# Kernel tuning notes

Measured on AMD Instinct MI355X. Metric: run time of the kernel, lower is better.

Reference implementation:

```python
import jax, jax.numpy as jnp
import numpy as np

B, S, N_WIRES, EMBED_DIM, NUM_HEADS = 4, 2048, 8, 512, 8
D_K = EMBED_DIM // NUM_HEADS


def setup_inputs() -> dict:
    key = jax.random.key(0)
    k_x, k_th, k_q, k_k, k_v, k_c = jax.random.split(key, 6)
    x = jax.random.normal(k_x, (B, S, N_WIRES), dtype=jnp.float32)
    # trainable RX rotation angles, one per wire
    theta = jax.random.normal(k_th, (N_WIRES,), dtype=jnp.float32) * 0.1
    # nn.Linear(n_wires, embed_dim, bias=False) weights have shape (embed_dim, n_wires)
    sc_in = 1.0 / np.sqrt(N_WIRES)
    Wq = jax.random.normal(k_q, (EMBED_DIM, N_WIRES), dtype=jnp.float32) * sc_in
    Wk = jax.random.normal(k_k, (EMBED_DIM, N_WIRES), dtype=jnp.float32) * sc_in
    Wv = jax.random.normal(k_v, (EMBED_DIM, N_WIRES), dtype=jnp.float32) * sc_in
    Wc = jax.random.normal(k_c, (EMBED_DIM, EMBED_DIM), dtype=jnp.float32) * (1.0 / np.sqrt(EMBED_DIM))
    return {"x": x, "theta": theta, "Wq": Wq, "Wk": Wk, "Wv": Wv, "Wc": Wc}


def reference(x, theta, Wq, Wk, Wv, Wc):
    # Quantum encoding closed form: RX(x_i) then RX(theta_i) on |0> per wire gives <Z> = cos(x_i + theta_i).
    proj = jnp.cos(x + theta)  # (B, S, n_wires)
    b, s, _ = proj.shape
    q = jnp.einsum('bsn,en->bse', proj, Wq)
    k = jnp.einsum('bsn,en->bse', proj, Wk)
    v = jnp.einsum('bsn,en->bse', proj, Wv)
    # split heads: (B, H, S, d_k)
    q = q.reshape(b, s, NUM_HEADS, D_K).transpose(0, 2, 1, 3)
    k = k.reshape(b, s, NUM_HEADS, D_K).transpose(0, 2, 1, 3)
    v = v.reshape(b, s, NUM_HEADS, D_K).transpose(0, 2, 1, 3)
    scores = jnp.einsum('bhqd,bhkd->bhqk', q, k) / np.sqrt(D_K).astype(np.float32)
    attn = jax.nn.softmax(scores, axis=-1)  # dropout is identity at inference
    out = jnp.einsum('bhqk,bhkd->bhqd', attn, v)
    out = out.transpose(0, 2, 1, 3).reshape(b, s, EMBED_DIM)
    return jnp.einsum('bse,fe->bsf', out, Wc)
```

## Files before the change

kernel.cpp:

```cpp
#include <hip/hip_runtime.h>
#include <stdint.h>

#define N_B 4
#define S_LEN 2048
#define N_H 8
#define E_DIM 512

typedef __attribute__((ext_vector_type(8))) short bf16x8;
typedef __attribute__((ext_vector_type(4))) float f32x4;
typedef __attribute__((ext_vector_type(4))) unsigned int u32x4;
typedef __attribute__((ext_vector_type(2))) unsigned int u32x2;
typedef __attribute__((ext_vector_type(4))) unsigned short u16x4;
typedef __attribute__((ext_vector_type(8))) unsigned short u16x8;

#define MFMA16(a, b, c) __builtin_amdgcn_mfma_f32_16x16x32_bf16((a), (b), (c), 0, 0, 0)

__device__ __forceinline__ unsigned short f2bf(float f) {
    union { float f; unsigned int u; } v; v.f = f;
    unsigned int r = v.u + 0x7fffu + ((v.u >> 16) & 1u);
    return (unsigned short)(r >> 16);
}

__device__ __forceinline__ unsigned int pack2bf(float lo, float hi) {
    union { float f; unsigned int u; } a, b; a.f = lo; b.f = hi;
    return __builtin_amdgcn_perm(b.u + 0x8000u, a.u + 0x8000u, 0x07060302u);
}

__device__ __forceinline__ float fexp2(float x) {
#if __has_builtin(__builtin_amdgcn_exp2f)
    return __builtin_amdgcn_exp2f(x);
#else
    return exp2f(x);
#endif
}

#if __has_builtin(__builtin_amdgcn_permlane32_swap) && __has_builtin(__builtin_amdgcn_permlane16_swap)
#define HAVE_PERMLANE_SWAP 1
#endif

__device__ __forceinline__ void pl32(unsigned int& x, unsigned int& y) {
#ifdef HAVE_PERMLANE_SWAP
    auto r = __builtin_amdgcn_permlane32_swap(x, y, false, false);
    x = (unsigned int)r[0]; y = (unsigned int)r[1];
#else
    const int idx = (((int)threadIdx.x & 63) ^ 32) << 2;
    unsigned int xs = (unsigned int)__builtin_amdgcn_ds_bpermute(idx, (int)x);
    unsigned int ys = (unsigned int)__builtin_amdgcn_ds_bpermute(idx, (int)y);
    const bool lo = (threadIdx.x & 32) == 0;
    unsigned int nx = lo ? x : ys;
    unsigned int ny = lo ? xs : y;
    x = nx; y = ny;
#endif
}

__device__ __forceinline__ void pl16(unsigned int& x, unsigned int& y) {
#ifdef HAVE_PERMLANE_SWAP
    auto r = __builtin_amdgcn_permlane16_swap(x, y, false, false);
    x = (unsigned int)r[0]; y = (unsigned int)r[1];
#else
    unsigned int zs = (unsigned int)__builtin_amdgcn_ds_swizzle((int)y, 0x401F);
    unsigned int ws = (unsigned int)__builtin_amdgcn_ds_swizzle((int)x, 0x401F);
    const bool evenq = (threadIdx.x & 16) == 0;
    unsigned int nx = evenq ? x : zs;
    unsigned int ny = evenq ? ws : y;
    x = nx; y = ny;
#endif
}

#define Q_SCALE 0.18033688f

__global__ __launch_bounds__(256) void qkv_kernel(
    const float* __restrict__ x, const float* __restrict__ theta,
    const float* __restrict__ Wq, const float* __restrict__ Wk,
    const float* __restrict__ Wv,
    unsigned short* __restrict__ Q, unsigned short* __restrict__ K,
    unsigned short* __restrict__ Vt)
{
    __shared__ float proj[32][8];
    const int tid = threadIdx.x;
    const int mat = blockIdx.x % 3;
    const int chunk = blockIdx.x / 3;
    const int row0 = chunk * 32;
    const int b = row0 >> 11;
    const int s_in_b = row0 & (S_LEN - 1);

    proj[tid >> 3][tid & 7] = cosf(x[row0 * 8 + tid] + theta[tid & 7]);
    __syncthreads();

    if (mat < 2) {
        const float* W = (mat == 0) ? Wq : Wk;
        const float scale = (mat == 0) ? Q_SCALE : 1.0f;
        unsigned short* outp = (mat == 0) ? Q : K;
        const int eg = (tid & 127) * 4;
        const int sg = (tid >> 7) * 16;
        float w[4][8];
        #pragma unroll
        for (int e = 0; e < 4; ++e)
            #pragma unroll
            for (int n = 0; n < 8; ++n)
                w[e][n] = W[(eg + e) * 8 + n] * scale;
        const int h = eg >> 6, d0 = eg & 63;
        unsigned short* p0 = outp + ((size_t)(b * N_H + h) * S_LEN + s_in_b + sg) * 64 + d0;
        #pragma unroll 4
        for (int s = 0; s < 16; ++s) {
            f32x4 pa = *(const f32x4*)&proj[sg + s][0];
            f32x4 pc = *(const f32x4*)&proj[sg + s][4];
            u16x4 o;
            #pragma unroll
            for (int e = 0; e < 4; ++e) {
                float a = 0.f;
                #pragma unroll
                for (int n = 0; n < 4; ++n)
                    a += pa[n] * w[e][n] + pc[n] * w[e][n + 4];
                o[e] = f2bf(a);
            }
            *(u16x4*)&p0[s * 64] = o;
        }
    } else {
        f32x4 ps[8][2];
        const int sl0 = (tid & 3) * 8;
        #pragma unroll
        for (int k2 = 0; k2 < 8; ++k2) {
            ps[k2][0] = *(const f32x4*)&proj[sl0 + k2][0];
            ps[k2][1] = *(const f32x4*)&proj[sl0 + k2][4];
        }
        const int ecol = tid >> 2;
        for (int pass = 0; pass < 8; ++pass) {
            const int e = pass * 64 + ecol;
            const int h = e >> 6, dd = e & 63;
            float wr[8];
            #pragma unroll
            for (int n = 0; n < 8; ++n) wr[n] = Wv[e * 8 + n];
            u16x8 pk;
            #pragma unroll
            for (int k2 = 0; k2 < 8; ++k2) {
                float acc = 0.f;
                #pragma unroll
                for (int n = 0; n < 4; ++n)
                    acc += ps[k2][0][n] * wr[n] + ps[k2][1][n] * wr[n + 4];
                pk[k2] = f2bf(acc);
            }
            *(u16x8*)&Vt[((size_t)(b * N_H + h) * 64 + dd) * S_LEN + s_in_b + sl0] = pk;
        }
    }
}

__global__ __launch_bounds__(256, 2) void flash_kernel(
    const unsigned short* __restrict__ Q, const unsigned short* __restrict__ K,
    const unsigned short* __restrict__ Vt, unsigned short* __restrict__ O)
{
    __shared__ short kt[2][64 * 72];
    __shared__ short vt[2][64 * 72];

    const int tid = threadIdx.x;
    const int lane = tid & 63, w = tid >> 6;
    const int quad = lane >> 4, lq = lane & 15;
    const int qt = blockIdx.x & 15, bh = blockIdx.x >> 4;
    const int b = bh >> 3, h = bh & 7;

    const unsigned short* Qb = Q + (size_t)bh * S_LEN * 64;
    const unsigned short* Kb = K + (size_t)bh * S_LEN * 64;
    const unsigned short* Vb = Vt + (size_t)bh * 64 * S_LEN;

    bf16x8 qf[2][2];
    #pragma unroll
    for (int mt = 0; mt < 2; ++mt)
        #pragma unroll
        for (int ks = 0; ks < 2; ++ks)
            qf[mt][ks] = *(const bf16x8*)&Qb[(size_t)(qt * 128 + w * 32 + mt * 16 + lq) * 64 + ks * 32 + quad * 8];

    f32x4 oacc[2][4];
    #pragma unroll
    for (int mt = 0; mt < 2; ++mt)
        #pragma unroll
        for (int dt = 0; dt < 4; ++dt) oacc[mt][dt] = 0.f;
    float lsum[2] = {0.f, 0.f};

    u32x4 pkr[2], pvr[2];
    #pragma unroll
    for (int i = 0; i < 2; ++i) {
        const int u = tid + (i << 8);
        pkr[i] = *(const u32x4*)&Kb[(size_t)(u >> 3) * 64 + (u & 7) * 8];
        pvr[i] = *(const u32x4*)&Vb[(size_t)(u >> 3) * S_LEN + (u & 7) * 8];
    }
    #pragma unroll
    for (int i = 0; i < 2; ++i) {
        const int u = tid + (i << 8);
        *(u32x4*)&kt[0][(u >> 3) * 72 + (u & 7) * 8] = pkr[i];
        *(u32x4*)&vt[0][(u >> 3) * 72 + (u & 7) * 8] = pvr[i];
    }
    #pragma unroll
    for (int i = 0; i < 2; ++i) {
        const int u = tid + (i << 8);
        pkr[i] = *(const u32x4*)&Kb[(size_t)(64 + (u >> 3)) * 64 + (u & 7) * 8];
        pvr[i] = *(const u32x4*)&Vb[(size_t)(u >> 3) * S_LEN + 64 + (u & 7) * 8];
    }
    asm volatile("s_waitcnt lgkmcnt(0)" ::: "memory");
    __builtin_amdgcn_s_barrier();

    for (int kti = 0; kti < 32; ++kti) {
        const int cur = kti & 1, nxt = cur ^ 1;

        #pragma unroll
        for (int i = 0; i < 2; ++i) {
            const int u = tid + (i << 8);
            *(u32x4*)&kt[nxt][(u >> 3) * 72 + (u & 7) * 8] = pkr[i];
            *(u32x4*)&vt[nxt][(u >> 3) * 72 + (u & 7) * 8] = pvr[i];
        }
        const int kb2 = (kti < 30) ? (kti + 2) * 64 : 0;
        #pragma unroll
        for (int i = 0; i < 2; ++i) {
            const int u = tid + (i << 8);
            pkr[i] = *(const u32x4*)&Kb[(size_t)(kb2 + (u >> 3)) * 64 + (u & 7) * 8];
            pvr[i] = *(const u32x4*)&Vb[(size_t)(u >> 3) * S_LEN + kb2 + (u & 7) * 8];
        }

        const short* ktc = &kt[cur][0];
        const short* vtc = &vt[cur][0];

        f32x4 sacc[2][4];
        #pragma unroll
        for (int mt = 0; mt < 2; ++mt)
            #pragma unroll
            for (int mts = 0; mts < 4; ++mts) sacc[mt][mts] = 0.f;
        #pragma unroll
        for (int mts = 0; mts < 4; ++mts) {
            #pragma unroll
            for (int ks = 0; ks < 2; ++ks) {
                bf16x8 af = *(const bf16x8*)&ktc[(mts * 16 + lq) * 72 + ks * 32 + quad * 8];
                sacc[0][mts] = MFMA16(af, qf[0][ks], sacc[0][mts]);
                sacc[1][mts] = MFMA16(af, qf[1][ks], sacc[1][mts]);
            }
        }

        unsigned int afr[2][2][4];
        #pragma unroll
        for (int mt = 0; mt < 2; ++mt) {
            unsigned int u[4][2];
            #pragma unroll
            for (int mts = 0; mts < 4; ++mts) {
                f32x4 p;
                #pragma unroll
                for (int e = 0; e < 4; ++e) p[e] = fexp2(sacc[mt][mts][e]);
                lsum[mt] += (p[0] + p[1]) + (p[2] + p[3]);
                u[mts][0] = pack2bf(p[0], p[1]);
                u[mts][1] = pack2bf(p[2], p[3]);
            }
            #pragma unroll
            for (int ks = 0; ks < 2; ++ks) {
                #pragma unroll
                for (int wd = 0; wd < 2; ++wd) {
                    unsigned int a = u[ks * 2][wd];
                    unsigned int c = u[ks * 2 + 1][wd];
                    pl32(a, c);
                    pl16(a, c);
                    afr[mt][ks][wd] = a;
                    afr[mt][ks][2 + wd] = c;
                }
            }
        }

        #pragma unroll
        for (int ks = 0; ks < 2; ++ks) {
            union { unsigned int u[4]; bf16x8 v; } a0, a1;
            #pragma unroll
            for (int j = 0; j < 4; ++j) { a0.u[j] = afr[0][ks][j]; a1.u[j] = afr[1][ks][j]; }
            #pragma unroll
            for (int dt = 0; dt < 4; ++dt) {
                bf16x8 bf = *(const bf16x8*)&vtc[(dt * 16 + lq) * 72 + ks * 32 + quad * 8];
                oacc[0][dt] = MFMA16(a0.v, bf, oacc[0][dt]);
                oacc[1][dt] = MFMA16(a1.v, bf, oacc[1][dt]);
            }
        }

        asm volatile("s_waitcnt lgkmcnt(0)" ::: "memory");
        __builtin_amdgcn_s_barrier();
    }

    #pragma unroll
    for (int mt = 0; mt < 2; ++mt) {
        float rs = lsum[mt];
        rs += __shfl_xor(rs, 16);
        rs += __shfl_xor(rs, 32);
        const float inv = 1.0f / rs;
        #pragma unroll
        for (int r = 0; r < 4; ++r) {
            const float ir = __shfl(inv, quad * 4 + r);
            const int row = qt * 128 + w * 32 + mt * 16 + quad * 4 + r;
            unsigned short* dst = &O[((size_t)b * S_LEN + row) * E_DIM + h * 64];
            #pragma unroll
            for (int dt = 0; dt < 4; ++dt)
                dst[dt * 16 + lq] = f2bf(oacc[mt][dt][r] * ir);
        }
    }
}

__global__ __launch_bounds__(256, 4) void outproj_kernel(
    const unsigned short* __restrict__ O, const float* __restrict__ Wc,
    float* __restrict__ Y)
{
    __shared__ short at[64 * 72];
    __shared__ short bt[64 * 72];
    const int tid = threadIdx.x;
    const int lane = tid & 63, w = tid >> 6;
    const int quad = lane >> 4, lq = lane & 15;
    const int m0 = (blockIdx.x >> 3) * 64;
    const int f0 = (blockIdx.x & 7) * 64;

    f32x4 acc[4];
    #pragma unroll
    for (int nt = 0; nt < 4; ++nt) acc[nt] = 0.f;

    u32x4 pa[2];
    f32x4 pw[4];
    #pragma unroll
    for (int i = 0; i < 2; ++i) {
        const int u = tid + (i << 8);
        pa[i] = *(const u32x4*)&O[(size_t)(m0 + (u >> 3)) * E_DIM + (u & 7) * 8];
    }
    #pragma unroll
    for (int i = 0; i < 4; ++i) {
        const int u = tid + (i << 8);
        pw[i] = *(const f32x4*)&Wc[(size_t)(f0 + (u >> 4)) * E_DIM + (u & 15) * 4];
    }

    for (int e0 = 0; e0 < E_DIM; e0 += 64) {
        __syncthreads();
        #pragma unroll
        for (int i = 0; i < 2; ++i) {
            const int u = tid + (i << 8);
            *(u32x4*)&at[(u >> 3) * 72 + (u & 7) * 8] = pa[i];
        }
        #pragma unroll
        for (int i = 0; i < 4; ++i) {
            const int u = tid + (i << 8);
            u16x4 pk = { f2bf(pw[i][0]), f2bf(pw[i][1]), f2bf(pw[i][2]), f2bf(pw[i][3]) };
            *(u16x4*)&bt[(u >> 4) * 72 + (u & 15) * 4] = pk;
        }
        __syncthreads();

        const int e1 = (e0 + 64 < E_DIM) ? e0 + 64 : 0;
        #pragma unroll
        for (int i = 0; i < 2; ++i) {
            const int u = tid + (i << 8);
            pa[i] = *(const u32x4*)&O[(size_t)(m0 + (u >> 3)) * E_DIM + e1 + (u & 7) * 8];
        }
        #pragma unroll
        for (int i = 0; i < 4; ++i) {
            const int u = tid + (i << 8);
            pw[i] = *(const f32x4*)&Wc[(size_t)(f0 + (u >> 4)) * E_DIM + e1 + (u & 15) * 4];
        }

        bf16x8 afk[2];
        #pragma unroll
        for (int ks = 0; ks < 2; ++ks)
            afk[ks] = *(const bf16x8*)&at[(w * 16 + lq) * 72 + ks * 32 + quad * 8];
        #pragma unroll
        for (int nt = 0; nt < 4; ++nt) {
            #pragma unroll
            for (int ks = 0; ks < 2; ++ks) {
                bf16x8 bf = *(const bf16x8*)&bt[(nt * 16 + lq) * 72 + ks * 32 + quad * 8];
                acc[nt] = MFMA16(afk[ks], bf, acc[nt]);
            }
        }
    }

    #pragma unroll
    for (int nt = 0; nt < 4; ++nt)
        #pragma unroll
        for (int r = 0; r < 4; ++r)
            Y[(size_t)(m0 + w * 16 + quad * 4 + r) * E_DIM + f0 + nt * 16 + lq] = acc[nt][r];
}

extern "C" void kernel_launch(void* const* d_in, const int* in_sizes, int n_in,
                              void* d_out, int out_size, void* d_ws, size_t ws_size,
                              hipStream_t stream) {
    const float* x     = (const float*)d_in[0];
    const float* theta = (const float*)d_in[1];
    const float* Wq    = (const float*)d_in[2];
    const float* Wk    = (const float*)d_in[3];
    const float* Wv    = (const float*)d_in[4];
    const float* Wc    = (const float*)d_in[5];
    float* Y = (float*)d_out;

    char* ws = (char*)d_ws;
    unsigned short* Q  = (unsigned short*)(ws);
    unsigned short* K  = (unsigned short*)(ws + ((size_t)8 << 20));
    unsigned short* Vt = (unsigned short*)(ws + ((size_t)16 << 20));
    unsigned short* O  = (unsigned short*)(ws + ((size_t)24 << 20));

    qkv_kernel<<<(N_B * S_LEN / 32) * 3, 256, 0, stream>>>(x, theta, Wq, Wk, Wv, Q, K, Vt);
    flash_kernel<<<N_B * N_H * (S_LEN / 128), 256, 0, stream>>>(Q, K, Vt, O);
    outproj_kernel<<<(N_B * S_LEN / 64) * (E_DIM / 64), 256, 0, stream>>>(O, Wc, Y);
}
```

Measured before the change: 140.1 us.

## Use 2-wave flash blocks with 64 query rows per wave and swizzled block order

The flash attention kernel moves from 4 waves with 32 query rows each to 2 waves with 64 query rows each. Each K/V fragment read from LDS now feeds four MFMAs instead of two, which cuts LDS traffic per FLOP. The key tile is processed in two 32-column halves to limit register pressure, and block IDs are remapped so that consecutive blocks spread across batch-heads. The cost is fewer waves per block, more accumulator registers and possibly lower occupancy, with each thread doing twice the global-to-LDS staging.

```diff
diff --git a/kernel.cpp b/kernel.cpp
--- a/kernel.cpp
+++ b/kernel.cpp
@@ -145,7 +145,7 @@
     }
 }
 
-__global__ __launch_bounds__(256, 2) void flash_kernel(
+__global__ __launch_bounds__(128) void flash_kernel(
     const unsigned short* __restrict__ Q, const unsigned short* __restrict__ K,
     const unsigned short* __restrict__ Vt, unsigned short* __restrict__ O)
 {
@@ -155,43 +155,44 @@
     const int tid = threadIdx.x;
     const int lane = tid & 63, w = tid >> 6;
     const int quad = lane >> 4, lq = lane & 15;
-    const int qt = blockIdx.x & 15, bh = blockIdx.x >> 4;
+    const int bid = (blockIdx.x & 7) * 64 + (blockIdx.x >> 3);
+    const int qt = bid & 15, bh = bid >> 4;
     const int b = bh >> 3, h = bh & 7;
 
     const unsigned short* Qb = Q + (size_t)bh * S_LEN * 64;
     const unsigned short* Kb = K + (size_t)bh * S_LEN * 64;
     const unsigned short* Vb = Vt + (size_t)bh * 64 * S_LEN;
 
-    bf16x8 qf[2][2];
-    #pragma unroll
-    for (int mt = 0; mt < 2; ++mt)
+    bf16x8 qf[4][2];
+    #pragma unroll
+    for (int mt = 0; mt < 4; ++mt)
         #pragma unroll
         for (int ks = 0; ks < 2; ++ks)
-            qf[mt][ks] = *(const bf16x8*)&Qb[(size_t)(qt * 128 + w * 32 + mt * 16 + lq) * 64 + ks * 32 + quad * 8];
-
-    f32x4 oacc[2][4];
-    #pragma unroll
-    for (int mt = 0; mt < 2; ++mt)
+            qf[mt][ks] = *(const bf16x8*)&Qb[(size_t)(qt * 128 + w * 64 + mt * 16 + lq) * 64 + ks * 32 + quad * 8];
+
+    f32x4 oacc[4][4];
+    #pragma unroll
+    for (int mt = 0; mt < 4; ++mt)
         #pragma unroll
         for (int dt = 0; dt < 4; ++dt) oacc[mt][dt] = 0.f;
-    float lsum[2] = {0.f, 0.f};
-
-    u32x4 pkr[2], pvr[2];
-    #pragma unroll
-    for (int i = 0; i < 2; ++i) {
-        const int u = tid + (i << 8);
+    float lsum[4] = {0.f, 0.f, 0.f, 0.f};
+
+    u32x4 pkr[4], pvr[4];
+    #pragma unroll
+    for (int i = 0; i < 4; ++i) {
+        const int u = tid + (i << 7);
         pkr[i] = *(const u32x4*)&Kb[(size_t)(u >> 3) * 64 + (u & 7) * 8];
         pvr[i] = *(const u32x4*)&Vb[(size_t)(u >> 3) * S_LEN + (u & 7) * 8];
     }
     #pragma unroll
-    for (int i = 0; i < 2; ++i) {
-        const int u = tid + (i << 8);
+    for (int i = 0; i < 4; ++i) {
+        const int u = tid + (i << 7);
         *(u32x4*)&kt[0][(u >> 3) * 72 + (u & 7) * 8] = pkr[i];
         *(u32x4*)&vt[0][(u >> 3) * 72 + (u & 7) * 8] = pvr[i];
     }
     #pragma unroll
-    for (int i = 0; i < 2; ++i) {
-        const int u = tid + (i << 8);
+    for (int i = 0; i < 4; ++i) {
+        const int u = tid + (i << 7);
         pkr[i] = *(const u32x4*)&Kb[(size_t)(64 + (u >> 3)) * 64 + (u & 7) * 8];
         pvr[i] = *(const u32x4*)&Vb[(size_t)(u >> 3) * S_LEN + 64 + (u & 7) * 8];
     }
@@ -202,15 +203,15 @@
         const int cur = kti & 1, nxt = cur ^ 1;
 
         #pragma unroll
-        for (int i = 0; i < 2; ++i) {
-            const int u = tid + (i << 8);
+        for (int i = 0; i < 4; ++i) {
+            const int u = tid + (i << 7);
             *(u32x4*)&kt[nxt][(u >> 3) * 72 + (u & 7) * 8] = pkr[i];
             *(u32x4*)&vt[nxt][(u >> 3) * 72 + (u & 7) * 8] = pvr[i];
         }
         const int kb2 = (kti < 30) ? (kti + 2) * 64 : 0;
         #pragma unroll
-        for (int i = 0; i < 2; ++i) {
-            const int u = tid + (i << 8);
+        for (int i = 0; i < 4; ++i) {
+            const int u = tid + (i << 7);
             pkr[i] = *(const u32x4*)&Kb[(size_t)(kb2 + (u >> 3)) * 64 + (u & 7) * 8];
             pvr[i] = *(const u32x4*)&Vb[(size_t)(u >> 3) * S_LEN + kb2 + (u & 7) * 8];
         }
@@ -218,58 +219,56 @@
         const short* ktc = &kt[cur][0];
         const short* vtc = &vt[cur][0];
 
-        f32x4 sacc[2][4];
-        #pragma unroll
-        for (int mt = 0; mt < 2; ++mt)
-            #pragma unroll
-            for (int mts = 0; mts < 4; ++mts) sacc[mt][mts] = 0.f;
-        #pragma unroll
-        for (int mts = 0; mts < 4; ++mts) {
-            #pragma unroll
-            for (int ks = 0; ks < 2; ++ks) {
-                bf16x8 af = *(const bf16x8*)&ktc[(mts * 16 + lq) * 72 + ks * 32 + quad * 8];
-                sacc[0][mts] = MFMA16(af, qf[0][ks], sacc[0][mts]);
-                sacc[1][mts] = MFMA16(af, qf[1][ks], sacc[1][mts]);
-            }
-        }
-
-        unsigned int afr[2][2][4];
-        #pragma unroll
-        for (int mt = 0; mt < 2; ++mt) {
-            unsigned int u[4][2];
-            #pragma unroll
-            for (int mts = 0; mts < 4; ++mts) {
-                f32x4 p;
-                #pragma unroll
-                for (int e = 0; e < 4; ++e) p[e] = fexp2(sacc[mt][mts][e]);
-                lsum[mt] += (p[0] + p[1]) + (p[2] + p[3]);
-                u[mts][0] = pack2bf(p[0], p[1]);
-                u[mts][1] = pack2bf(p[2], p[3]);
-            }
-            #pragma unroll
-            for (int ks = 0; ks < 2; ++ks) {
+        #pragma unroll
+        for (int ksub = 0; ksub < 2; ++ksub) {
+            f32x4 sacc[4][2];
+            #pragma unroll
+            for (int mt = 0; mt < 4; ++mt)
+                #pragma unroll
+                for (int m2 = 0; m2 < 2; ++m2) sacc[mt][m2] = 0.f;
+            #pragma unroll
+            for (int m2 = 0; m2 < 2; ++m2) {
+                #pragma unroll
+                for (int ks = 0; ks < 2; ++ks) {
+                    bf16x8 af = *(const bf16x8*)&ktc[((ksub * 2 + m2) * 16 + lq) * 72 + ks * 32 + quad * 8];
+                    #pragma unroll
+                    for (int mt = 0; mt < 4; ++mt)
+                        sacc[mt][m2] = MFMA16(af, qf[mt][ks], sacc[mt][m2]);
+                }
+            }
+
+            bf16x8 pa[4];
+            #pragma unroll
+            for (int mt = 0; mt < 4; ++mt) {
+                unsigned int u_[2][2];
+                #pragma unroll
+                for (int m2 = 0; m2 < 2; ++m2) {
+                    f32x4 p;
+                    #pragma unroll
+                    for (int e = 0; e < 4; ++e) p[e] = fexp2(sacc[mt][m2][e]);
+                    lsum[mt] += (p[0] + p[1]) + (p[2] + p[3]);
+                    u_[m2][0] = pack2bf(p[0], p[1]);
+                    u_[m2][1] = pack2bf(p[2], p[3]);
+                }
+                union { unsigned int uu[4]; bf16x8 v; } A;
                 #pragma unroll
                 for (int wd = 0; wd < 2; ++wd) {
-                    unsigned int a = u[ks * 2][wd];
-                    unsigned int c = u[ks * 2 + 1][wd];
+                    unsigned int a = u_[0][wd];
+                    unsigned int c = u_[1][wd];
                     pl32(a, c);
                     pl16(a, c);
-                    afr[mt][ks][wd] = a;
-                    afr[mt][ks][2 + wd] = c;
+                    A.uu[wd] = a;
+                    A.uu[2 + wd] = c;
                 }
-            }
-        }
-
-        #pragma unroll
-        for (int ks = 0; ks < 2; ++ks) {
-            union { unsigned int u[4]; bf16x8 v; } a0, a1;
-            #pragma unroll
-            for (int j = 0; j < 4; ++j) { a0.u[j] = afr[0][ks][j]; a1.u[j] = afr[1][ks][j]; }
+                pa[mt] = A.v;
+            }
+
             #pragma unroll
             for (int dt = 0; dt < 4; ++dt) {
-                bf16x8 bf = *(const bf16x8*)&vtc[(dt * 16 + lq) * 72 + ks * 32 + quad * 8];
-                oacc[0][dt] = MFMA16(a0.v, bf, oacc[0][dt]);
-                oacc[1][dt] = MFMA16(a1.v, bf, oacc[1][dt]);
+                bf16x8 bf = *(const bf16x8*)&vtc[(dt * 16 + lq) * 72 + ksub * 32 + quad * 8];
+                #pragma unroll
+                for (int mt = 0; mt < 4; ++mt)
+                    oacc[mt][dt] = MFMA16(pa[mt], bf, oacc[mt][dt]);
             }
         }
 
@@ -278,7 +277,7 @@
     }
 
     #pragma unroll
-    for (int mt = 0; mt < 2; ++mt) {
+    for (int mt = 0; mt < 4; ++mt) {
         float rs = lsum[mt];
         rs += __shfl_xor(rs, 16);
         rs += __shfl_xor(rs, 32);
@@ -286,7 +285,7 @@
         #pragma unroll
         for (int r = 0; r < 4; ++r) {
             const float ir = __shfl(inv, quad * 4 + r);
-            const int row = qt * 128 + w * 32 + mt * 16 + quad * 4 + r;
+            const int row = qt * 128 + w * 64 + mt * 16 + quad * 4 + r;
             unsigned short* dst = &O[((size_t)b * S_LEN + row) * E_DIM + h * 64];
             #pragma unroll
             for (int dt = 0; dt < 4; ++dt)
@@ -390,6 +389,6 @@
     unsigned short* O  = (unsigned short*)(ws + ((size_t)24 << 20));
 
     qkv_kernel<<<(N_B * S_LEN / 32) * 3, 256, 0, stream>>>(x, theta, Wq, Wk, Wv, Q, K, Vt);
-    flash_kernel<<<N_B * N_H * (S_LEN / 128), 256, 0, stream>>>(Q, K, Vt, O);
+    flash_kernel<<<N_B * N_H * (S_LEN / 128), 128, 0, stream>>>(Q, K, Vt, O);
     outproj_kernel<<<(N_B * S_LEN / 64) * (E_DIM / 64), 256, 0, stream>>>(O, Wc, Y);
 }
```

Result: slower. 153.5 us (+9.5%).

## Split flash attention KV range across two warp groups and merge via LDS

Applied to the files above, without the earlier changes.

Doubles the flash kernel's block to 512 threads. Two groups of four waves each process half of the key sequence for the same 128 query rows, and their partial output and row-sum accumulators are reduced through shared memory at the end. Block indices are also remapped so that neighbouring blocks fall on different heads. This targets low occupancy and parallelism, since only 512 blocks ran before. It costs doubled LDS for the K/V buffers plus a final barrier and reduction. The reduction is valid because no running max is tracked (plain exp2 sums), so the two partial sums can simply be added.

```diff
diff --git a/kernel.cpp b/kernel.cpp
--- a/kernel.cpp
+++ b/kernel.cpp
@@ -145,29 +145,34 @@
     }
 }
 
-__global__ __launch_bounds__(256, 2) void flash_kernel(
+__global__ __launch_bounds__(512, 4) void flash_kernel(
     const unsigned short* __restrict__ Q, const unsigned short* __restrict__ K,
     const unsigned short* __restrict__ Vt, unsigned short* __restrict__ O)
 {
-    __shared__ short kt[2][64 * 72];
-    __shared__ short vt[2][64 * 72];
+    __shared__ short kt[2][2][64 * 72];
+    __shared__ short vt[2][2][64 * 72];
 
     const int tid = threadIdx.x;
     const int lane = tid & 63, w = tid >> 6;
+    const int g = tid >> 8;
+    const int wq = w & 3;
+    const int tg = tid & 255;
     const int quad = lane >> 4, lq = lane & 15;
-    const int qt = blockIdx.x & 15, bh = blockIdx.x >> 4;
+    const int bid = (blockIdx.x & 7) * 64 + (blockIdx.x >> 3);
+    const int qt = bid & 15, bh = bid >> 4;
     const int b = bh >> 3, h = bh & 7;
 
     const unsigned short* Qb = Q + (size_t)bh * S_LEN * 64;
     const unsigned short* Kb = K + (size_t)bh * S_LEN * 64;
     const unsigned short* Vb = Vt + (size_t)bh * 64 * S_LEN;
+    const int kbase = g * 1024;
 
     bf16x8 qf[2][2];
     #pragma unroll
     for (int mt = 0; mt < 2; ++mt)
         #pragma unroll
         for (int ks = 0; ks < 2; ++ks)
-            qf[mt][ks] = *(const bf16x8*)&Qb[(size_t)(qt * 128 + w * 32 + mt * 16 + lq) * 64 + ks * 32 + quad * 8];
+            qf[mt][ks] = *(const bf16x8*)&Qb[(size_t)(qt * 128 + wq * 32 + mt * 16 + lq) * 64 + ks * 32 + quad * 8];
 
     f32x4 oacc[2][4];
     #pragma unroll
@@ -179,44 +184,44 @@
     u32x4 pkr[2], pvr[2];
     #pragma unroll
     for (int i = 0; i < 2; ++i) {
-        const int u = tid + (i << 8);
-        pkr[i] = *(const u32x4*)&Kb[(size_t)(u >> 3) * 64 + (u & 7) * 8];
-        pvr[i] = *(const u32x4*)&Vb[(size_t)(u >> 3) * S_LEN + (u & 7) * 8];
+        const int u = tg + (i << 8);
+        pkr[i] = *(const u32x4*)&Kb[(size_t)(kbase + (u >> 3)) * 64 + (u & 7) * 8];
+        pvr[i] = *(const u32x4*)&Vb[(size_t)(u >> 3) * S_LEN + kbase + (u & 7) * 8];
     }
     #pragma unroll
     for (int i = 0; i < 2; ++i) {
-        const int u = tid + (i << 8);
-        *(u32x4*)&kt[0][(u >> 3) * 72 + (u & 7) * 8] = pkr[i];
-        *(u32x4*)&vt[0][(u >> 3) * 72 + (u & 7) * 8] = pvr[i];
+        const int u = tg + (i << 8);
+        *(u32x4*)&kt[g][0][(u >> 3) * 72 + (u & 7) * 8] = pkr[i];
+        *(u32x4*)&vt[g][0][(u >> 3) * 72 + (u & 7) * 8] = pvr[i];
     }
     #pragma unroll
     for (int i = 0; i < 2; ++i) {
-        const int u = tid + (i << 8);
-        pkr[i] = *(const u32x4*)&Kb[(size_t)(64 + (u >> 3)) * 64 + (u & 7) * 8];
-        pvr[i] = *(const u32x4*)&Vb[(size_t)(u >> 3) * S_LEN + 64 + (u & 7) * 8];
+        const int u = tg + (i << 8);
+        pkr[i] = *(const u32x4*)&Kb[(size_t)(kbase + 64 + (u >> 3)) * 64 + (u & 7) * 8];
+        pvr[i] = *(const u32x4*)&Vb[(size_t)(u >> 3) * S_LEN + kbase + 64 + (u & 7) * 8];
     }
     asm volatile("s_waitcnt lgkmcnt(0)" ::: "memory");
     __builtin_amdgcn_s_barrier();
 
-    for (int kti = 0; kti < 32; ++kti) {
+    for (int kti = 0; kti < 16; ++kti) {
         const int cur = kti & 1, nxt = cur ^ 1;
 
         #pragma unroll
         for (int i = 0; i < 2; ++i) {
-            const int u = tid + (i << 8);
-            *(u32x4*)&kt[nxt][(u >> 3) * 72 + (u & 7) * 8] = pkr[i];
-            *(u32x4*)&vt[nxt][(u >> 3) * 72 + (u & 7) * 8] = pvr[i];
-        }
-        const int kb2 = (kti < 30) ? (kti + 2) * 64 : 0;
+            const int u = tg + (i << 8);
+            *(u32x4*)&kt[g][nxt][(u >> 3) * 72 + (u & 7) * 8] = pkr[i];
+            *(u32x4*)&vt[g][nxt][(u >> 3) * 72 + (u & 7) * 8] = pvr[i];
+        }
+        const int kb2 = kbase + ((kti < 14) ? (kti + 2) * 64 : 0);
         #pragma unroll
         for (int i = 0; i < 2; ++i) {
-            const int u = tid + (i << 8);
+            const int u = tg + (i << 8);
             pkr[i] = *(const u32x4*)&Kb[(size_t)(kb2 + (u >> 3)) * 64 + (u & 7) * 8];
             pvr[i] = *(const u32x4*)&Vb[(size_t)(u >> 3) * S_LEN + kb2 + (u & 7) * 8];
         }
 
-        const short* ktc = &kt[cur][0];
-        const short* vtc = &vt[cur][0];
+        const short* ktc = &kt[g][cur][0];
+        const short* vtc = &vt[g][cur][0];
 
         f32x4 sacc[2][4];
         #pragma unroll
@@ -236,22 +241,22 @@
         unsigned int afr[2][2][4];
         #pragma unroll
         for (int mt = 0; mt < 2; ++mt) {
-            unsigned int u[4][2];
+            unsigned int u_[4][2];
             #pragma unroll
             for (int mts = 0; mts < 4; ++mts) {
                 f32x4 p;
                 #pragma unroll
                 for (int e = 0; e < 4; ++e) p[e] = fexp2(sacc[mt][mts][e]);
                 lsum[mt] += (p[0] + p[1]) + (p[2] + p[3]);
-                u[mts][0] = pack2bf(p[0], p[1]);
-                u[mts][1] = pack2bf(p[2], p[3]);
+                u_[mts][0] = pack2bf(p[0], p[1]);
+                u_[mts][1] = pack2bf(p[2], p[3]);
             }
             #pragma unroll
             for (int ks = 0; ks < 2; ++ks) {
                 #pragma unroll
                 for (int wd = 0; wd < 2; ++wd) {
-                    unsigned int a = u[ks * 2][wd];
-                    unsigned int c = u[ks * 2 + 1][wd];
+                    unsigned int a = u_[ks * 2][wd];
+                    unsigned int c = u_[ks * 2 + 1][wd];
                     pl32(a, c);
                     pl16(a, c);
                     afr[mt][ks][wd] = a;
@@ -277,20 +282,44 @@
         __builtin_amdgcn_s_barrier();
     }
 
-    #pragma unroll
-    for (int mt = 0; mt < 2; ++mt) {
-        float rs = lsum[mt];
-        rs += __shfl_xor(rs, 16);
-        rs += __shfl_xor(rs, 32);
-        const float inv = 1.0f / rs;
-        #pragma unroll
-        for (int r = 0; r < 4; ++r) {
-            const float ir = __shfl(inv, quad * 4 + r);
-            const int row = qt * 128 + w * 32 + mt * 16 + quad * 4 + r;
-            unsigned short* dst = &O[((size_t)b * S_LEN + row) * E_DIM + h * 64];
+    float* exO = (float*)&kt[0][0][0];
+    float* exL = (float*)&vt[0][0][0];
+    if (g == 1) {
+        const int fb = wq * 2304 + lane * 36;
+        #pragma unroll
+        for (int mt = 0; mt < 2; ++mt)
             #pragma unroll
             for (int dt = 0; dt < 4; ++dt)
-                dst[dt * 16 + lq] = f2bf(oacc[mt][dt][r] * ir);
+                *(f32x4*)&exO[fb + (mt * 4 + dt) * 4] = oacc[mt][dt];
+        exL[(wq * 64 + lane) * 2 + 0] = lsum[0];
+        exL[(wq * 64 + lane) * 2 + 1] = lsum[1];
+    }
+    __syncthreads();
+    if (g == 0) {
+        const int fb = wq * 2304 + lane * 36;
+        #pragma unroll
+        for (int mt = 0; mt < 2; ++mt)
+            #pragma unroll
+            for (int dt = 0; dt < 4; ++dt)
+                oacc[mt][dt] += *(const f32x4*)&exO[fb + (mt * 4 + dt) * 4];
+        lsum[0] += exL[(wq * 64 + lane) * 2 + 0];
+        lsum[1] += exL[(wq * 64 + lane) * 2 + 1];
+
+        #pragma unroll
+        for (int mt = 0; mt < 2; ++mt) {
+            float rs = lsum[mt];
+            rs += __shfl_xor(rs, 16);
+            rs += __shfl_xor(rs, 32);
+            const float inv = 1.0f / rs;
+            #pragma unroll
+            for (int r = 0; r < 4; ++r) {
+                const float ir = __shfl(inv, quad * 4 + r);
+                const int row = qt * 128 + wq * 32 + mt * 16 + quad * 4 + r;
+                unsigned short* dst = &O[((size_t)b * S_LEN + row) * E_DIM + h * 64];
+                #pragma unroll
+                for (int dt = 0; dt < 4; ++dt)
+                    dst[dt * 16 + lq] = f2bf(oacc[mt][dt][r] * ir);
+            }
         }
     }
 }
@@ -390,6 +419,6 @@
     unsigned short* O  = (unsigned short*)(ws + ((size_t)24 << 20));
 
     qkv_kernel<<<(N_B * S_LEN / 32) * 3, 256, 0, stream>>>(x, theta, Wq, Wk, Wv, Q, K, Vt);
-    flash_kernel<<<N_B * N_H * (S_LEN / 128), 256, 0, stream>>>(Q, K, Vt, O);
+    flash_kernel<<<N_B * N_H * (S_LEN / 128), 512, 0, stream>>>(Q, K, Vt, O);
     outproj_kernel<<<(N_B * S_LEN / 64) * (E_DIM / 64), 256, 0, stream>>>(O, Wc, Y);
 }
```

Result: no change. 137.4 us (-2.0%).
